# Optimization experiments

Measured on AMD Instinct MI355X. Metric: run time of the kernel, lower is better.

The kernel has to match this reference:

```python
import jax, jax.numpy as jnp
import numpy as np

# ---- static config (mirrors DRR.__init__ kwargs) ----
NX = NY = NZ = 192            # volume dims
H = W = 192                   # detector height/width
SDR = 300.0                   # source-to-rotation-center distance
DELX = DELY = 2.0             # detector pixel pitch (mm)
X0 = Y0 = 0.0                 # detector offsets
SPACING = (1.0, 1.0, 1.0)     # voxel spacing (mm)
BAM = 1.0                     # bone_attenuation_multiplier
B = 2                         # batch (poses)
N_SUB = H * W // 2            # p_subsample = 0.5


def setup_inputs() -> dict:
    key = jax.random.key(0)
    k1, k2, k3, k4 = jax.random.split(key, 4)
    # CT volume in Hounsfield units, spanning air (-1000) to bone (~2000)
    volume = jax.random.uniform(k1, (NX, NY, NZ), jnp.float32, -1000.0, 2000.0)
    rotations = jax.random.normal(k2, (B, 3), jnp.float32)          # Euler ZYX (rad)
    translations = jax.random.normal(k3, (B, 3), jnp.float32) * 10.0  # mm, near isocenter
    # unique subsampled detector pixel indices (Detector.subsamples[-1])
    subsample_idx = jax.random.permutation(k4, H * W)[:N_SUB].astype(jnp.int32)
    return {"volume": volume, "rotations": rotations,
            "translations": translations, "subsample_idx": subsample_idx}


def _rz(t):
    c, s = jnp.cos(t), jnp.sin(t); z = jnp.zeros_like(t); o = jnp.ones_like(t)
    return jnp.stack([jnp.stack([c, -s, z], -1),
                      jnp.stack([s, c, z], -1),
                      jnp.stack([z, z, o], -1)], -2)


def _ry(t):
    c, s = jnp.cos(t), jnp.sin(t); z = jnp.zeros_like(t); o = jnp.ones_like(t)
    return jnp.stack([jnp.stack([c, z, s], -1),
                      jnp.stack([z, o, z], -1),
                      jnp.stack([-s, z, c], -1)], -2)


def _rx(t):
    c, s = jnp.cos(t), jnp.sin(t); z = jnp.zeros_like(t); o = jnp.ones_like(t)
    return jnp.stack([jnp.stack([o, z, z], -1),
                      jnp.stack([z, c, -s], -1),
                      jnp.stack([z, s, c], -1)], -2)


def _density(volume):
    # DRR.__init__: volume.flip([0]); air/soft/bone HU segmentation + normalization
    vol = jnp.flip(volume, 0)
    soft = (vol > -800.0) & (vol <= 350.0)
    soft_min = jnp.min(jnp.where(soft, vol, jnp.inf))
    d = jnp.where(vol <= -800.0, soft_min,
                  jnp.where(vol > 350.0, vol * BAM, vol))
    d = d - jnp.min(d)
    return d / jnp.max(d)


def _canonical_detector():
    # source on +z at SDR, detector plane at -z; pixel grid with pitch delx/dely
    xs = (jnp.arange(W, dtype=jnp.float32) - (W - 1) / 2.0) * DELX + X0
    ys = (jnp.arange(H, dtype=jnp.float32) - (H - 1) / 2.0) * DELY + Y0
    gy, gx = jnp.meshgrid(ys, xs, indexing="ij")
    tgt = jnp.stack([gx.ravel(), gy.ravel(),
                     jnp.full((H * W,), -SDR, jnp.float32)], -1)  # [H*W, 3]
    src = jnp.array([0.0, 0.0, SDR], jnp.float32)
    return src, tgt


def _siddon(density, source, target):
    """Siddon ray-casting. source [B,3], target [B,N,3] -> line integrals [B,N]."""
    dims = density.shape
    sp = jnp.asarray(SPACING, density.dtype)
    src = source[:, None, :]                     # [B,1,3]
    sdd = target - src                           # [B,N,3]
    sdd_safe = jnp.where(sdd == 0, 1e-9, sdd)
    # parametric intersections with all grid planes per axis
    alist = [(jnp.arange(dims[a] + 1, dtype=density.dtype)[None, None, :] * sp[a]
              - src[..., a:a + 1]) / sdd_safe[..., a:a + 1] for a in range(3)]
    a_first = jnp.stack([al[..., 0] for al in alist], -1)    # [B,N,3]
    a_last = jnp.stack([al[..., -1] for al in alist], -1)
    amin = jnp.maximum(jnp.max(jnp.minimum(a_first, a_last), -1), 0.0)[..., None]
    amax = jnp.minimum(jnp.min(jnp.maximum(a_first, a_last), -1), 1.0)[..., None]
    amax = jnp.maximum(amax, amin)               # ray misses -> zero-length segments
    alphas = jnp.sort(jnp.clip(jnp.concatenate(alist, -1), amin, amax), -1)  # [B,N,M+1]
    mid = 0.5 * (alphas[..., 1:] + alphas[..., :-1])                         # [B,N,M]
    ray_len = jnp.linalg.norm(target - src, axis=-1, keepdims=True)
    step = (alphas[..., 1:] - alphas[..., :-1]) * ray_len                    # [B,N,M]
    pts = src[..., None, :] + mid[..., None] * sdd[..., None, :]             # [B,N,M,3]
    idx = jnp.clip(jnp.floor(pts / sp).astype(jnp.int32), 0,
                   jnp.array(dims, jnp.int32) - 1)
    vox = density[idx[..., 0], idx[..., 1], idx[..., 2]]                     # gather
    return jnp.sum(step * vox, -1)


def reference(volume, rotations, translations, subsample_idx):
    density = _density(volume)
    src_c, tgt_c = _canonical_detector()
    tgt_c = tgt_c[subsample_idx]                                  # [N,3] subsampled rays
    R = _rz(rotations[:, 0]) @ _ry(rotations[:, 1]) @ _rx(rotations[:, 2])  # [B,3,3]
    center = jnp.array([NX, NY, NZ], jnp.float32) * jnp.asarray(SPACING, jnp.float32) / 2.0
    t = translations + center                                     # pose about isocenter
    source = jnp.einsum("bij,j->bi", R, src_c) + t                # [B,3]
    target = jnp.einsum("bij,nj->bni", R, tgt_c) + t[:, None, :]  # [B,N,3]
    img = _siddon(density, source, target)                        # [B,N]
    # reshape_subsampled_drr: scatter into zeros [B, H*W] then view [B,1,H,W]
    drr = jnp.zeros((img.shape[0], H * W), img.dtype).at[:, subsample_idx].set(img)
    return drr.reshape(-1, 1, H, W)
```

## Files before the change

kernel.cpp:

```cpp
#include <hip/hip_runtime.h>
#include <float.h>
#include <math.h>


#define NDIM   192
#define HW     (NDIM * NDIM)
#define NSUB   (HW / 2)
#define NTILE  576
#define NBATCH 2
#define NCHUNK 16
#define NVOX   (NDIM * NDIM * NDIM)
#define SDRF   300.0f
#define RBLK   1728
#define NBLKX  (NSUB / 256)

#define WS_LIST_OFF 16
#define WS_PART_OFF (WS_LIST_OFF + 4 * NSUB)

__global__ __launch_bounds__(256) void reduce_kernel(
    const float* __restrict__ vol, float* __restrict__ parts) {
    const int tid = blockIdx.x * 256 + threadIdx.x;
    const float4* __restrict__ v4 = (const float4*)vol;
    const int S = RBLK * 256;

    float4 r0 = v4[tid + 0 * S];
    float4 r1 = v4[tid + 1 * S];
    float4 r2 = v4[tid + 2 * S];
    float4 r3 = v4[tid + 3 * S];

    float smin = FLT_MAX, rmin = FLT_MAX, rmax = -FLT_MAX;
    float4 rr[4] = {r0, r1, r2, r3};
#pragma unroll
    for (int k = 0; k < 4; ++k) {
        float xs[4] = {rr[k].x, rr[k].y, rr[k].z, rr[k].w};
#pragma unroll
        for (int j = 0; j < 4; ++j) {
            float x = xs[j];
            bool in = (x > -800.0f);
            rmin = fminf(rmin, in ? x : FLT_MAX);
            rmax = fmaxf(rmax, in ? x : -FLT_MAX);
            smin = fminf(smin, (in && x <= 350.0f) ? x : FLT_MAX);
        }
    }
#pragma unroll
    for (int off = 32; off > 0; off >>= 1) {
        smin = fminf(smin, __shfl_down(smin, off));
        rmin = fminf(rmin, __shfl_down(rmin, off));
        rmax = fmaxf(rmax, __shfl_down(rmax, off));
    }
    __shared__ float sm[4], rm[4], rx[4];
    int w = threadIdx.x >> 6;
    if ((threadIdx.x & 63) == 0) { sm[w] = smin; rm[w] = rmin; rx[w] = rmax; }
    __syncthreads();
    if (threadIdx.x == 0) {
        parts[blockIdx.x] =
            fminf(fminf(sm[0], sm[1]), fminf(sm[2], sm[3]));
        parts[RBLK + blockIdx.x] =
            fminf(fminf(rm[0], rm[1]), fminf(rm[2], rm[3]));
        parts[2 * RBLK + blockIdx.x] =
            fmaxf(fmaxf(rx[0], rx[1]), fmaxf(rx[2], rx[3]));
    }
}

__global__ __launch_bounds__(1024) void prep_kernel(
    const float* __restrict__ parts, const int* __restrict__ sidx,
    float* __restrict__ ws, int* __restrict__ list) {
    __shared__ unsigned int bits[HW / 32];
    __shared__ int cnts[NTILE];
    __shared__ float red0[16], red1[16], red2[16];

    const int tid = threadIdx.x;

    float smin = FLT_MAX, rmin = FLT_MAX, rmax = -FLT_MAX;
    for (int i = tid; i < RBLK; i += 1024) {
        smin = fminf(smin, parts[i]);
        rmin = fminf(rmin, parts[RBLK + i]);
        rmax = fmaxf(rmax, parts[2 * RBLK + i]);
    }
#pragma unroll
    for (int off = 32; off > 0; off >>= 1) {
        smin = fminf(smin, __shfl_down(smin, off));
        rmin = fminf(rmin, __shfl_down(rmin, off));
        rmax = fmaxf(rmax, __shfl_down(rmax, off));
    }
    int w = tid >> 6;
    if ((tid & 63) == 0) { red0[w] = smin; red1[w] = rmin; red2[w] = rmax; }

    for (int i = tid; i < HW / 32; i += 1024) bits[i] = 0u;
    __syncthreads();
    if (tid == 0) {
        float a = FLT_MAX, b = FLT_MAX, c = -FLT_MAX;
#pragma unroll
        for (int k = 0; k < 16; ++k) {
            a = fminf(a, red0[k]);
            b = fminf(b, red1[k]);
            c = fmaxf(c, red2[k]);
        }
        ws[0] = a; ws[1] = b; ws[2] = c;
    }

    for (int i = tid; i < NSUB; i += 1024) {
        int p = sidx[i];
        atomicOr(&bits[p >> 5], 1u << (p & 31));
    }
    __syncthreads();

    const unsigned char* bb = (const unsigned char*)bits;
    int myc = 0;
    int ti = tid / 24, tj = tid % 24;
    if (tid < NTILE) {
#pragma unroll
        for (int r = 0; r < 8; ++r)
            myc += __popc((int)bb[(ti * 8 + r) * 24 + tj]);
        cnts[tid] = myc;
    }
    __syncthreads();

    for (int off = 1; off < NTILE; off <<= 1) {
        int v = 0, u = 0;
        if (tid < NTILE) {
            v = cnts[tid];
            if (tid >= off) u = cnts[tid - off];
        }
        __syncthreads();
        if (tid < NTILE) cnts[tid] = v + u;
        __syncthreads();
    }

    if (tid < NTILE) {
        int o = cnts[tid] - myc;
#pragma unroll
        for (int r = 0; r < 8; ++r) {
            int pibase = (ti * 8 + r) * NDIM + tj * 8;
            unsigned int m = (unsigned int)bb[(ti * 8 + r) * 24 + tj];
            while (m) {
                int j = __ffs(m) - 1;
                m &= m - 1u;
                list[o++] = pibase + j;
            }
        }
    }
}

__device__ __forceinline__ void init_axis(float s, float d, float a_lo,
                                          int& i, int& st, float& na) {
    if (d > 0.0f) {
        st = 1;
        float f = s + a_lo * d;
        int ii = (int)floorf(f) + 1;
        ii = max(0, min(ii, NDIM + 1));
        while (ii <= NDIM && ((float)ii - s) / d <= a_lo) ++ii;
        while (ii > 0 && ((float)(ii - 1) - s) / d > a_lo) --ii;
        i  = ii;
        na = (ii <= NDIM) ? ((float)ii - s) / d : FLT_MAX;
    } else {
        st = -1;
        float f = s + a_lo * d;
        int ii = (int)ceilf(f) - 1;
        ii = max(-1, min(ii, NDIM));
        while (ii >= 0 && ((float)ii - s) / d <= a_lo) --ii;
        while (ii < NDIM && ((float)(ii + 1) - s) / d > a_lo) ++ii;
        i  = ii;
        na = (ii >= 0) ? ((float)ii - s) / d : FLT_MAX;
    }
}

__global__ __launch_bounds__(256) void ray_kernel(
    const float* __restrict__ vol, const float* __restrict__ rot,
    const float* __restrict__ trans, const float* __restrict__ wsc,
    const int* __restrict__ list, float* __restrict__ out) {
    const int c = blockIdx.y;
    const int b = blockIdx.z;

    const int n = blockIdx.x * 256 + threadIdx.x;
    const int p  = list[n];
    const int pi = p / NDIM;
    const int pj = p % NDIM;

    float smin = wsc[0];
    float rmin = wsc[1];
    float rmax = wsc[2];
    float dmin = fminf(smin, rmin);
    float dmax = fmaxf(smin, rmax);
    float scale = 1.0f / (dmax - dmin);

    float rz = rot[b * 3 + 0], ry = rot[b * 3 + 1], rx = rot[b * 3 + 2];
    float cz = cosf(rz), sz = sinf(rz);
    float cy = cosf(ry), sy = sinf(ry);
    float cx = cosf(rx), sx = sinf(rx);
    float R00 = cz * cy;
    float R01 = cz * sy * sx - sz * cx;
    float R02 = sz * sx + cz * sy * cx;
    float R10 = sz * cy;
    float R11 = cz * cx + sz * sy * sx;
    float R12 = sz * sy * cx - cz * sx;
    float R20 = -sy;
    float R21 = cy * sx;
    float R22 = cy * cx;
    float tx = trans[b * 3 + 0] + 96.0f;
    float ty = trans[b * 3 + 1] + 96.0f;
    float tz = trans[b * 3 + 2] + 96.0f;

    float srcx = R02 * SDRF + tx;
    float srcy = R12 * SDRF + ty;
    float srcz = R22 * SDRF + tz;
    float gx = ((float)pj - 95.5f) * 2.0f;
    float gy = ((float)pi - 95.5f) * 2.0f;
    float tgx = R00 * gx + R01 * gy + R02 * (-SDRF) + tx;
    float tgy = R10 * gx + R11 * gy + R12 * (-SDRF) + ty;
    float tgz = R20 * gx + R21 * gy + R22 * (-SDRF) + tz;

    float sdx = tgx - srcx, sdy = tgy - srcy, sdz = tgz - srcz;
    float dsx = (sdx == 0.0f) ? 1e-9f : sdx;
    float dsy = (sdy == 0.0f) ? 1e-9f : sdy;
    float dsz = (sdz == 0.0f) ? 1e-9f : sdz;

    float af0 = (0.0f - srcx) / dsx, al0 = (192.0f - srcx) / dsx;
    float af1 = (0.0f - srcy) / dsy, al1 = (192.0f - srcy) / dsy;
    float af2 = (0.0f - srcz) / dsz, al2 = (192.0f - srcz) / dsz;
    float amin = fmaxf(fmaxf(fminf(af0, al0), fminf(af1, al1)), fminf(af2, al2));
    amin = fmaxf(amin, 0.0f);
    float amax = fminf(fminf(fmaxf(af0, al0), fmaxf(af1, al1)), fmaxf(af2, al2));
    amax = fminf(amax, 1.0f);
    amax = fmaxf(amax, amin);
    float ray_len = sqrtf(sdx * sdx + sdy * sdy + sdz * sdz);

    float span = amax - amin;
    float a_lo = amin + span * ((float)c / (float)NCHUNK);
    float a_hi = (c == NCHUNK - 1) ? amax
                                   : amin + span * ((float)(c + 1) / (float)NCHUNK);

    int i0, i1, i2, st0, st1, st2;
    float na0, na1, na2;
    init_axis(srcx, dsx, a_lo, i0, st0, na0);
    init_axis(srcy, dsy, a_lo, i1, st1, na1);
    init_axis(srcz, dsz, a_lo, i2, st2, na2);

    float r0 = 1.0f / dsx, r1 = 1.0f / dsy, r2 = 1.0f / dsz;
    float mr0 = -srcx * r0, mr1 = -srcy * r1, mr2 = -srcz * r2;
    float fi0 = (float)i0, fi1 = (float)i1, fi2 = (float)i2;
    float fs0 = (float)st0, fs1 = (float)st1, fs2 = (float)st2;

    int T = 1;
    if (na0 < a_hi) T += (int)((a_hi - na0) * fabsf(dsx)) + 2;
    if (na1 < a_hi) T += (int)((a_hi - na1) * fabsf(dsy)) + 2;
    if (na2 < a_hi) T += (int)((a_hi - na2) * fabsf(dsz)) + 2;

    float cur = a_lo;
    float acc = 0.0f;

    auto ADV = [&](float& wseg, int& addr) {
        float an = fminf(fminf(na0, na1), na2);
        float ae = fminf(an, a_hi);
        wseg = ae - cur;
        float mid = 0.5f * (cur + ae);
        float px = fmaf(mid, sdx, srcx);
        float py = fmaf(mid, sdy, srcy);
        float pz = fmaf(mid, sdz, srcz);
        int ix = min(max((int)px, 0), NDIM - 1);
        int iy = min(max((int)py, 0), NDIM - 1);
        int iz = min(max((int)pz, 0), NDIM - 1);
        addr = (NDIM - 1) * HW - ix * HW + iy * NDIM + iz;
        cur = ae;
        bool c0 = (na0 == an), c1 = (na1 == an), c2 = (na2 == an);
        float nf0 = fi0 + fs0, nf1 = fi1 + fs1, nf2 = fi2 + fs2;
        float nn0 = fmaf(nf0, r0, mr0);
        float nn1 = fmaf(nf1, r1, mr1);
        float nn2 = fmaf(nf2, r2, mr2);
        fi0 = c0 ? nf0 : fi0;  na0 = c0 ? nn0 : na0;
        fi1 = c1 ? nf1 : fi1;  na1 = c1 ? nn1 : na1;
        fi2 = c2 ? nf2 : fi2;  na2 = c2 ? nn2 : na2;
    };

    float w0s, w1s, w2s, w3s, w4s, w5s, w6s, w7s;
    int   ad0, ad1, ad2, ad3, ad4, ad5, ad6, ad7;
    float v0, v1, v2, v3, v4, v5, v6, v7;
    ADV(w0s, ad0); v0 = vol[ad0];
    ADV(w1s, ad1); v1 = vol[ad1];
    ADV(w2s, ad2); v2 = vol[ad2];
    ADV(w3s, ad3); v3 = vol[ad3];
    ADV(w4s, ad4); v4 = vol[ad4];
    ADV(w5s, ad5); v5 = vol[ad5];
    ADV(w6s, ad6); v6 = vol[ad6];
    ADV(w7s, ad7); v7 = vol[ad7];

#define SLOT_STEP(W, A, V)                        \
    {                                             \
        float dv = ((V) <= -800.0f) ? smin : (V); \
        acc = fmaf((W), dv, acc);                 \
        ADV((W), (A));                            \
        (V) = vol[(A)];                           \
    }

    for (int s = 0; s < T; s += 8) {
        SLOT_STEP(w0s, ad0, v0);
        SLOT_STEP(w1s, ad1, v1);
        SLOT_STEP(w2s, ad2, v2);
        SLOT_STEP(w3s, ad3, v3);
        SLOT_STEP(w4s, ad4, v4);
        SLOT_STEP(w5s, ad5, v5);
        SLOT_STEP(w6s, ad6, v6);
        SLOT_STEP(w7s, ad7, v7);
    }
#undef SLOT_STEP

    float res = (acc - dmin * (a_hi - a_lo)) * scale * ray_len;
    atomicAdd(&out[b * HW + p], res);
}

extern "C" void kernel_launch(void* const* d_in, const int* in_sizes, int n_in,
                              void* d_out, int out_size, void* d_ws,
                              size_t ws_size, hipStream_t stream) {
    const float* vol   = (const float*)d_in[0];
    const float* rot   = (const float*)d_in[1];
    const float* trans = (const float*)d_in[2];
    const int*   sidx  = (const int*)d_in[3];
    float* out = (float*)d_out;

    float* wsf   = (float*)d_ws;
    int*   list  = (int*)((unsigned char*)d_ws + WS_LIST_OFF);
    float* parts = (float*)((unsigned char*)d_ws + WS_PART_OFF);

    hipMemsetAsync(d_out, 0, (size_t)out_size * sizeof(float), stream);

    reduce_kernel<<<RBLK, 256, 0, stream>>>(vol, parts);
    prep_kernel<<<1, 1024, 0, stream>>>(parts, sidx, wsf, list);
    dim3 rgrid(NBLKX, NCHUNK, NBATCH);
    ray_kernel<<<rgrid, 256, 0, stream>>>(vol, rot, trans, wsf, list, out);
}
```

Baseline: 128.5 us.

## Order ray list center-out, shrink prefetch pipeline to 4 slots, use fmax clamp

The prep kernel now ranks the detector tiles by Chebyshev distance from the detector center, so the compacted ray list is emitted center-first. Neighbouring rays then tend to have similar lengths and volume footprints, which evens out per-wavefront trip counts and cache locality. The Siddon loop's software-pipelined gather depth drops from 8 to 4 slots, cutting register pressure at the cost of less memory-latency hiding. The air-replacement select becomes fmaxf(v, smin), which assumes smin is greater than -800 and that every value at or below -800 should map to smin, and that any value between -800 and smin is also clamped to it.

```diff
diff --git a/kernel.cpp b/kernel.cpp
--- a/kernel.cpp
+++ b/kernel.cpp
@@ -67,6 +67,7 @@
     float* __restrict__ ws, int* __restrict__ list) {
     __shared__ unsigned int bits[HW / 32];
     __shared__ int cnts[NTILE];
+    __shared__ int skey[NTILE];
     __shared__ float red0[16], red1[16], red2[16];
 
     const int tid = threadIdx.x;
@@ -106,13 +107,22 @@
     __syncthreads();
 
     const unsigned char* bb = (const unsigned char*)bits;
-    int myc = 0;
+    int myc = 0, myrank = 0;
     int ti = tid / 24, tj = tid % 24;
     if (tid < NTILE) {
 #pragma unroll
         for (int r = 0; r < 8; ++r)
             myc += __popc((int)bb[(ti * 8 + r) * 24 + tj]);
-        cnts[tid] = myc;
+        int d2i = max(abs(2 * ti - 23), abs(2 * tj - 23));
+        skey[tid] = d2i * 1024 + tid;
+    }
+    __syncthreads();
+    if (tid < NTILE) {
+        int k = skey[tid];
+        int rk = 0;
+        for (int t = 0; t < NTILE; ++t) rk += (skey[t] < k);
+        myrank = rk;
+        cnts[rk] = myc;
     }
     __syncthreads();
 
@@ -128,7 +138,7 @@
     }
 
     if (tid < NTILE) {
-        int o = cnts[tid] - myc;
+        int o = cnts[myrank] - myc;
 #pragma unroll
         for (int r = 0; r < 8; ++r) {
             int pibase = (ti * 8 + r) * NDIM + tj * 8;
@@ -272,35 +282,26 @@
         fi2 = c2 ? nf2 : fi2;  na2 = c2 ? nn2 : na2;
     };
 
-    float w0s, w1s, w2s, w3s, w4s, w5s, w6s, w7s;
-    int   ad0, ad1, ad2, ad3, ad4, ad5, ad6, ad7;
-    float v0, v1, v2, v3, v4, v5, v6, v7;
+    float w0s, w1s, w2s, w3s;
+    int   ad0, ad1, ad2, ad3;
+    float v0, v1, v2, v3;
     ADV(w0s, ad0); v0 = vol[ad0];
     ADV(w1s, ad1); v1 = vol[ad1];
     ADV(w2s, ad2); v2 = vol[ad2];
     ADV(w3s, ad3); v3 = vol[ad3];
-    ADV(w4s, ad4); v4 = vol[ad4];
-    ADV(w5s, ad5); v5 = vol[ad5];
-    ADV(w6s, ad6); v6 = vol[ad6];
-    ADV(w7s, ad7); v7 = vol[ad7];
-
-#define SLOT_STEP(W, A, V)                        \
-    {                                             \
-        float dv = ((V) <= -800.0f) ? smin : (V); \
-        acc = fmaf((W), dv, acc);                 \
-        ADV((W), (A));                            \
-        (V) = vol[(A)];                           \
-    }
-
-    for (int s = 0; s < T; s += 8) {
+
+#define SLOT_STEP(W, A, V)                         \
+    {                                              \
+        acc = fmaf((W), fmaxf((V), smin), acc);    \
+        ADV((W), (A));                             \
+        (V) = vol[(A)];                            \
+    }
+
+    for (int s = 0; s < T; s += 4) {
         SLOT_STEP(w0s, ad0, v0);
         SLOT_STEP(w1s, ad1, v1);
         SLOT_STEP(w2s, ad2, v2);
         SLOT_STEP(w3s, ad3, v3);
-        SLOT_STEP(w4s, ad4, v4);
-        SLOT_STEP(w5s, ad5, v5);
-        SLOT_STEP(w6s, ad6, v6);
-        SLOT_STEP(w7s, ad7, v7);
     }
 #undef SLOT_STEP
 
```

Result: slower. 138.1 us (+7.5%).
